# Optimization experiments

Measured on AMD Instinct MI355X. Metric: run time of the kernel, lower is better.

Reference implementation:

```python
import jax, jax.numpy as jnp
import numpy as np

B, N, IDIM, ODIM = 4096, 32, 1024, 1024


def setup_inputs() -> dict:
    key = jax.random.key(0)
    k1, k2, k3 = jax.random.split(key, 3)
    x = jax.random.normal(k1, (B, IDIM), dtype=jnp.float32)
    weight = jax.random.normal(k2, (N, ODIM, IDIM), dtype=jnp.float32)
    gate_w = jax.random.normal(k3, (N, IDIM), dtype=jnp.float32) * (1.0 / np.sqrt(IDIM))
    gate_b = jnp.zeros((N,), dtype=jnp.float32)
    return {"x": x, "weight": weight, "gate_w": gate_w, "gate_b": gate_b}


def reference(x, weight, gate_w, gate_b):
    # per-expert projection: [b, n, odim] (the large intermediate the torch code
    # materializes via einsum 'noi,biz->bnoz' with z=1)
    y = jnp.einsum('noi,bi->bno', weight, x)
    # gate weights: gelu(Linear(idim -> n)) ; torch gelu default is exact (erf)
    g = jax.nn.gelu(x @ gate_w.T + gate_b, approximate=False)  # [b, n]
    # gated combine over experts (the `y @ g` step after rearrange)
    out = jnp.einsum('bno,bn->bo', y, g)  # [b, odim]
    return out
```

## Files before the change

kernel.cpp:

```cpp
#include <hip/hip_runtime.h>
#include <hip/hip_bf16.h>
#include <math.h>


#define BSZ  4096
#define NEXP 32
#define IDIM 1024
#define ODIM 1024

typedef __attribute__((ext_vector_type(8))) short bf16x8;
typedef __attribute__((ext_vector_type(4))) float f32x4;

#define GLOAD_LDS16(g, l) __builtin_amdgcn_global_load_lds( \
    (const __attribute__((address_space(1))) void*)(g),     \
    (__attribute__((address_space(3))) void*)(l), 16, 0, 0)

#define SBAR __builtin_amdgcn_sched_barrier(0)
#define WAITV6 asm volatile("s_waitcnt vmcnt(6)" ::: "memory")
#define WAITV0 asm volatile("s_waitcnt vmcnt(0)" ::: "memory")

__device__ __forceinline__ unsigned short f2bf(float f) {
  unsigned u = __float_as_uint(f);
  unsigned r = (u + 0x7FFFu + ((u >> 16) & 1u)) >> 16;
  return (unsigned short)r;
}

__global__ void zero_kernel(float* __restrict__ out) {
  int i = blockIdx.x * blockDim.x + threadIdx.x;
  ((float4*)out)[i] = make_float4(0.f, 0.f, 0.f, 0.f);
}

__global__ void conv_kernel(const float* __restrict__ in, unsigned short* __restrict__ outb) {
  int i = blockIdx.x * blockDim.x + threadIdx.x;
  const float4* p = (const float4*)in + (size_t)i * 2;
  float4 a = p[0], b = p[1];
  union { bf16x8 v; unsigned short s[8]; } o;
  o.s[0] = f2bf(a.x); o.s[1] = f2bf(a.y); o.s[2] = f2bf(a.z); o.s[3] = f2bf(a.w);
  o.s[4] = f2bf(b.x); o.s[5] = f2bf(b.y); o.s[6] = f2bf(b.z); o.s[7] = f2bf(b.w);
  ((bf16x8*)outb)[i] = o.v;
}

__global__ void gate_kernel(const float* __restrict__ x, const float* __restrict__ gw,
                            const float* __restrict__ gb, float* __restrict__ gT) {
  const int lane = threadIdx.x & 63;
  const int row = blockIdx.x * 4 + (threadIdx.x >> 6);
  const float4* xr = (const float4*)(x + (size_t)row * IDIM);
  float4 xv[4];
#pragma unroll
  for (int t = 0; t < 4; ++t) xv[t] = xr[t * 64 + lane];
  for (int n = 0; n < NEXP; ++n) {
    const float4* wr = (const float4*)(gw + (size_t)n * IDIM);
    float s = 0.f;
#pragma unroll
    for (int t = 0; t < 4; ++t) {
      float4 wv = wr[t * 64 + lane];
      s += xv[t].x * wv.x + xv[t].y * wv.y + xv[t].z * wv.z + xv[t].w * wv.w;
    }
#pragma unroll
    for (int off = 32; off > 0; off >>= 1) s += __shfl_down(s, off, 64);
    if (lane == 0) {
      float v = s + gb[n];
      gT[(size_t)n * BSZ + row] = 0.5f * v * (1.0f + erff(v * 0.70710678118f));
    }
  }
}

__global__ __launch_bounds__(512, 2) void gemm_kernel(
    const unsigned short* __restrict__ xb,
    const unsigned short* __restrict__ wb,
    const float* __restrict__ gT,
    float* __restrict__ out)
{
  __shared__ unsigned short As[3][256 * 64];
  __shared__ unsigned short Bs[3][128 * 64];
  __shared__ float g_lds[16][256];

  const int tid  = threadIdx.x;
  const int lane = tid & 63;
  const int wid  = tid >> 6;
  const int wm   = wid >> 1;
  const int wn   = wid & 1;

  const int orig  = blockIdx.x;
  const int wgid  = (orig & 7) * 32 + (orig >> 3);
  const int mtile = wgid & 15;
  const int grp   = wgid >> 4;
  const int split = grp & 1;
  const int col0  = (grp >> 1) * 128;
  const int row0  = mtile * 256;

  const int srow = lane >> 3;
  const int jsrc = (lane & 7) ^ srow;
  size_t a_off[4], b_off[2];
#pragma unroll
  for (int l = 0; l < 4; ++l)
    a_off[l] = (size_t)(row0 + (wid * 4 + l) * 8 + srow) * IDIM + jsrc * 8;
#pragma unroll
  for (int l = 0; l < 2; ++l)
    b_off[l] = (size_t)(col0 + (wid * 2 + l) * 8 + srow) * IDIM + jsrc * 8;

  const int frow = lane & 15;
  const int hi   = lane >> 4;

  f32x4 acc[4][4], acc_e[4][4];
#pragma unroll
  for (int i = 0; i < 4; ++i)
#pragma unroll
    for (int j = 0; j < 4; ++j) {
      acc[i][j]   = f32x4{0.f, 0.f, 0.f, 0.f};
      acc_e[i][j] = f32x4{0.f, 0.f, 0.f, 0.f};
    }

  {
    const int e = tid >> 5;
    const int r = (tid & 31) * 8;
    const float* src = gT + ((size_t)(split * 16 + e) << 12) + row0 + r;
    *(float4*)&g_lds[e][r]     = *(const float4*)src;
    *(float4*)&g_lds[e][r + 4] = *(const float4*)(src + 4);
  }

  auto STAGE = [&](int buf, int kt) {
    const int e  = kt >> 4;
    const int i0 = (kt & 15) << 6;
    const unsigned short* wb_n = wb + ((size_t)(split * 16 + e) << 20);
#pragma unroll
    for (int l = 0; l < 4; ++l)
      GLOAD_LDS16(xb + a_off[l] + i0, &As[buf][(wid * 4 + l) * 512]);
#pragma unroll
    for (int l = 0; l < 2; ++l)
      GLOAD_LDS16(wb_n + b_off[l] + i0, &Bs[buf][(wid * 2 + l) * 512]);
  };

  __syncthreads();
  STAGE(0, 0);
  STAGE(1, 1);

  int cur = 0;
#pragma unroll 1
  for (int kt = 0; kt < 256; ++kt) {
    if (kt == 255) { WAITV0; } else { WAITV6; }
    SBAR;
    __builtin_amdgcn_s_barrier();
    SBAR;

    if (kt < 254) { int s = cur + 2; if (s >= 3) s -= 3; STAGE(s, kt + 2); }

    const unsigned short* A_ = &As[cur][0];
    const unsigned short* B_ = &Bs[cur][0];
    const int g0 = hi ^ (frow & 7);
    const int g1 = (4 + hi) ^ (frow & 7);

    bf16x8 af0[4], bf0[4];
#pragma unroll
    for (int ni = 0; ni < 4; ++ni)
      bf0[ni] = *(const bf16x8*)&B_[(wn * 64 + ni * 16 + frow) * 64 + g0 * 8];
#pragma unroll
    for (int mi = 0; mi < 4; ++mi)
      af0[mi] = *(const bf16x8*)&A_[(wm * 64 + mi * 16 + frow) * 64 + g0 * 8];
#pragma unroll
    for (int mi = 0; mi < 4; ++mi)
#pragma unroll
      for (int ni = 0; ni < 4; ++ni)
        acc_e[mi][ni] = __builtin_amdgcn_mfma_f32_16x16x32_bf16(
            af0[mi], bf0[ni], acc_e[mi][ni], 0, 0, 0);

    bf16x8 af1[4], bf1[4];
#pragma unroll
    for (int ni = 0; ni < 4; ++ni)
      bf1[ni] = *(const bf16x8*)&B_[(wn * 64 + ni * 16 + frow) * 64 + g1 * 8];
#pragma unroll
    for (int mi = 0; mi < 4; ++mi)
      af1[mi] = *(const bf16x8*)&A_[(wm * 64 + mi * 16 + frow) * 64 + g1 * 8];
#pragma unroll
    for (int mi = 0; mi < 4; ++mi)
#pragma unroll
      for (int ni = 0; ni < 4; ++ni)
        acc_e[mi][ni] = __builtin_amdgcn_mfma_f32_16x16x32_bf16(
            af1[mi], bf1[ni], acc_e[mi][ni], 0, 0, 0);

    if ((kt & 15) == 15) {
      const int e = kt >> 4;
#pragma unroll
      for (int mi = 0; mi < 4; ++mi) {
        float4 gv = *(const float4*)&g_lds[e][wm * 64 + mi * 16 + hi * 4];
        f32x4 g4 = f32x4{gv.x, gv.y, gv.z, gv.w};
#pragma unroll
        for (int ni = 0; ni < 4; ++ni) {
          acc[mi][ni] += g4 * acc_e[mi][ni];
          acc_e[mi][ni] = f32x4{0.f, 0.f, 0.f, 0.f};
        }
      }
    }
    if (++cur == 3) cur = 0;
  }

  const int orow0 = row0 + wm * 64 + hi * 4;
  const int ocol0 = col0 + wn * 64 + frow;
#pragma unroll
  for (int mi = 0; mi < 4; ++mi)
#pragma unroll
    for (int j = 0; j < 4; ++j) {
      const int r = orow0 + mi * 16 + j;
#pragma unroll
      for (int ni = 0; ni < 4; ++ni)
        atomicAdd(out + (size_t)r * ODIM + ocol0 + ni * 16, acc[mi][ni][j]);
    }
}

extern "C" void kernel_launch(void* const* d_in, const int* in_sizes, int n_in,
                              void* d_out, int out_size, void* d_ws, size_t ws_size,
                              hipStream_t stream) {
  const float* x  = (const float*)d_in[0];
  const float* w  = (const float*)d_in[1];
  const float* gw = (const float*)d_in[2];
  const float* gb = (const float*)d_in[3];
  float* out = (float*)d_out;

  unsigned short* xb   = (unsigned short*)d_ws;
  unsigned short* wbuf = (unsigned short*)((char*)d_ws + (8u << 20));
  float*          gT   = (float*)((char*)d_ws + (72u << 20));

  zero_kernel<<<(BSZ * ODIM / 4) / 256, 256, 0, stream>>>(out);
  conv_kernel<<<(BSZ * IDIM / 8) / 256, 256, 0, stream>>>(x, xb);
  conv_kernel<<<(NEXP * ODIM * IDIM / 8) / 256, 256, 0, stream>>>(w, wbuf);
  gate_kernel<<<BSZ / 4, 256, 0, stream>>>(x, gw, gb, gT);

  gemm_kernel<<<256, 512, 0, stream>>>(xb, wbuf, gT, out);
}
```

Baseline: 419.7 us.

## Load weight fragments directly from global to registers, drop LDS staging for B

The B (weight) tile is no longer staged through LDS. Each wave now loads its bf16 weight fragments straight from global memory into registers every k-step, while the A (activation) tile keeps its triple-buffered global-to-LDS pipeline, now with a vmcnt(4) wait. The change also drops the occupancy hint to one workgroup per CU, adds s_setprio around the MFMA block, and moves the barrier to the end of each iteration. The goal is to cut LDS traffic and LDS capacity for B. In exchange, global-load latency is exposed directly in the loop, and weight fetches are no longer shared between the wm-waves that use the same B columns.

```diff
diff --git a/kernel.cpp b/kernel.cpp
--- a/kernel.cpp
+++ b/kernel.cpp
@@ -8,6 +8,7 @@
 #define IDIM 1024
 #define ODIM 1024
 
+typedef unsigned short u16;
 typedef __attribute__((ext_vector_type(8))) short bf16x8;
 typedef __attribute__((ext_vector_type(4))) float f32x4;
 
@@ -16,13 +17,13 @@
     (__attribute__((address_space(3))) void*)(l), 16, 0, 0)
 
 #define SBAR __builtin_amdgcn_sched_barrier(0)
-#define WAITV6 asm volatile("s_waitcnt vmcnt(6)" ::: "memory")
-#define WAITV0 asm volatile("s_waitcnt vmcnt(0)" ::: "memory")
-
-__device__ __forceinline__ unsigned short f2bf(float f) {
+#define WAITV4 do { asm volatile("s_waitcnt vmcnt(4)" ::: "memory"); SBAR; } while (0)
+#define WAITV0 do { asm volatile("s_waitcnt vmcnt(0)" ::: "memory"); SBAR; } while (0)
+#define BARRIER __builtin_amdgcn_s_barrier()
+
+__device__ __forceinline__ u16 f2bf(float f) {
   unsigned u = __float_as_uint(f);
-  unsigned r = (u + 0x7FFFu + ((u >> 16) & 1u)) >> 16;
-  return (unsigned short)r;
+  return (u16)((u + 0x7FFFu + ((u >> 16) & 1u)) >> 16);
 }
 
 __global__ void zero_kernel(float* __restrict__ out) {
@@ -30,11 +31,11 @@
   ((float4*)out)[i] = make_float4(0.f, 0.f, 0.f, 0.f);
 }
 
-__global__ void conv_kernel(const float* __restrict__ in, unsigned short* __restrict__ outb) {
+__global__ void conv_kernel(const float* __restrict__ in, u16* __restrict__ outb) {
   int i = blockIdx.x * blockDim.x + threadIdx.x;
   const float4* p = (const float4*)in + (size_t)i * 2;
   float4 a = p[0], b = p[1];
-  union { bf16x8 v; unsigned short s[8]; } o;
+  union { bf16x8 v; u16 s[8]; } o;
   o.s[0] = f2bf(a.x); o.s[1] = f2bf(a.y); o.s[2] = f2bf(a.z); o.s[3] = f2bf(a.w);
   o.s[4] = f2bf(b.x); o.s[5] = f2bf(b.y); o.s[6] = f2bf(b.z); o.s[7] = f2bf(b.w);
   ((bf16x8*)outb)[i] = o.v;
@@ -65,14 +66,13 @@
   }
 }
 
-__global__ __launch_bounds__(512, 2) void gemm_kernel(
-    const unsigned short* __restrict__ xb,
-    const unsigned short* __restrict__ wb,
+__global__ __launch_bounds__(512, 1) void gemm_kernel(
+    const u16* __restrict__ xb,
+    const u16* __restrict__ wb,
     const float* __restrict__ gT,
     float* __restrict__ out)
 {
-  __shared__ unsigned short As[3][256 * 64];
-  __shared__ unsigned short Bs[3][128 * 64];
+  __shared__ u16 As[3][256 * 64];
   __shared__ float g_lds[16][256];
 
   const int tid  = threadIdx.x;
@@ -91,16 +91,16 @@
 
   const int srow = lane >> 3;
   const int jsrc = (lane & 7) ^ srow;
-  size_t a_off[4], b_off[2];
+  size_t a_off[4];
 #pragma unroll
   for (int l = 0; l < 4; ++l)
     a_off[l] = (size_t)(row0 + (wid * 4 + l) * 8 + srow) * IDIM + jsrc * 8;
-#pragma unroll
-  for (int l = 0; l < 2; ++l)
-    b_off[l] = (size_t)(col0 + (wid * 2 + l) * 8 + srow) * IDIM + jsrc * 8;
 
   const int frow = lane & 15;
   const int hi   = lane >> 4;
+  const int fs   = frow & 7;
+
+  const size_t bbase = (size_t)(col0 + wn * 64 + frow) * IDIM + hi * 8;
 
   f32x4 acc[4][4], acc_e[4][4];
 #pragma unroll
@@ -119,67 +119,55 @@
     *(float4*)&g_lds[e][r + 4] = *(const float4*)(src + 4);
   }
 
-  auto STAGE = [&](int buf, int kt) {
-    const int e  = kt >> 4;
-    const int i0 = (kt & 15) << 6;
-    const unsigned short* wb_n = wb + ((size_t)(split * 16 + e) << 20);
+  auto STAGE_A = [&](int buf, int kt) {
+    const size_t i0 = (size_t)((kt & 15) << 6);
 #pragma unroll
     for (int l = 0; l < 4; ++l)
       GLOAD_LDS16(xb + a_off[l] + i0, &As[buf][(wid * 4 + l) * 512]);
-#pragma unroll
-    for (int l = 0; l < 2; ++l)
-      GLOAD_LDS16(wb_n + b_off[l] + i0, &Bs[buf][(wid * 2 + l) * 512]);
   };
 
+  const int NKT = 256;
+
+  STAGE_A(0, 0);
+  STAGE_A(1, 1);
+  WAITV4;
   __syncthreads();
-  STAGE(0, 0);
-  STAGE(1, 1);
 
   int cur = 0;
 #pragma unroll 1
-  for (int kt = 0; kt < 256; ++kt) {
-    if (kt == 255) { WAITV0; } else { WAITV6; }
-    SBAR;
-    __builtin_amdgcn_s_barrier();
-    SBAR;
-
-    if (kt < 254) { int s = cur + 2; if (s >= 3) s -= 3; STAGE(s, kt + 2); }
-
-    const unsigned short* A_ = &As[cur][0];
-    const unsigned short* B_ = &Bs[cur][0];
-    const int g0 = hi ^ (frow & 7);
-    const int g1 = (4 + hi) ^ (frow & 7);
-
-    bf16x8 af0[4], bf0[4];
+  for (int kt = 0; kt < NKT; ++kt) {
+    const int e = kt >> 4;
+    const u16* wp = wb + (((size_t)(split * 16 + e)) << 20) + ((kt & 15) << 6) + bbase;
+    bf16x8 bfr[4][2];
 #pragma unroll
     for (int ni = 0; ni < 4; ++ni)
-      bf0[ni] = *(const bf16x8*)&B_[(wn * 64 + ni * 16 + frow) * 64 + g0 * 8];
+#pragma unroll
+      for (int kk = 0; kk < 2; ++kk)
+        bfr[ni][kk] = *(const bf16x8*)(wp + ni * 16 * IDIM + kk * 32);
+
+    if (kt + 2 < NKT) { int s = cur + 2; if (s >= 3) s -= 3; STAGE_A(s, kt + 2); }
+
+    bf16x8 af[4][2];
 #pragma unroll
     for (int mi = 0; mi < 4; ++mi)
-      af0[mi] = *(const bf16x8*)&A_[(wm * 64 + mi * 16 + frow) * 64 + g0 * 8];
+#pragma unroll
+      for (int kk = 0; kk < 2; ++kk)
+        af[mi][kk] = *(const bf16x8*)&As[cur][(wm * 64 + mi * 16 + frow) * 64 + (((kk << 2) + hi) ^ fs) * 8];
+
+    if (kt + 2 < NKT) { WAITV4; } else { WAITV0; }
+
+    __builtin_amdgcn_s_setprio(1);
 #pragma unroll
     for (int mi = 0; mi < 4; ++mi)
 #pragma unroll
       for (int ni = 0; ni < 4; ++ni)
-        acc_e[mi][ni] = __builtin_amdgcn_mfma_f32_16x16x32_bf16(
-            af0[mi], bf0[ni], acc_e[mi][ni], 0, 0, 0);
-
-    bf16x8 af1[4], bf1[4];
-#pragma unroll
-    for (int ni = 0; ni < 4; ++ni)
-      bf1[ni] = *(const bf16x8*)&B_[(wn * 64 + ni * 16 + frow) * 64 + g1 * 8];
-#pragma unroll
-    for (int mi = 0; mi < 4; ++mi)
-      af1[mi] = *(const bf16x8*)&A_[(wm * 64 + mi * 16 + frow) * 64 + g1 * 8];
-#pragma unroll
-    for (int mi = 0; mi < 4; ++mi)
-#pragma unroll
-      for (int ni = 0; ni < 4; ++ni)
-        acc_e[mi][ni] = __builtin_amdgcn_mfma_f32_16x16x32_bf16(
-            af1[mi], bf1[ni], acc_e[mi][ni], 0, 0, 0);
+#pragma unroll
+        for (int kk = 0; kk < 2; ++kk)
+          acc_e[mi][ni] = __builtin_amdgcn_mfma_f32_16x16x32_bf16(
+              af[mi][kk], bfr[ni][kk], acc_e[mi][ni], 0, 0, 0);
+    __builtin_amdgcn_s_setprio(0);
 
     if ((kt & 15) == 15) {
-      const int e = kt >> 4;
 #pragma unroll
       for (int mi = 0; mi < 4; ++mi) {
         float4 gv = *(const float4*)&g_lds[e][wm * 64 + mi * 16 + hi * 4];
@@ -191,6 +179,8 @@
         }
       }
     }
+
+    BARRIER;
     if (++cur == 3) cur = 0;
   }
 
```

Measured after the change: 759.5 us. +81.0%, slower.
